# Kernel optimization log

Hardware: AMD Instinct MI355X
Metric: run time of the kernel (lower is better)

## Reference

```python
import jax, jax.numpy as jnp
import numpy as np

B, S, D = 1, 2048, 2048      # batch, seq, hidden_dim
DF = 768                      # moe intermediate (per routed expert)
DSH = 2048                    # shared-expert intermediate
E, K = 32, 8                  # num routed experts, top_k
BLK = 128                     # fp8 block-scale size
CAP = 1024
T = B * S


def _dequant(w, s, blk=BLK):
    # w: [E, M, N] fp8 values (stored fp32), s: [E, M/blk, N/blk] block scales
    Eh, M, N = w.shape
    Mb, Nb = s.shape[1], s.shape[2]
    return (w.reshape(Eh, Mb, blk, Nb, blk) * s[:, :, None, :, None]).reshape(Eh, M, N)


def setup_inputs() -> dict:
    key = jax.random.key(0)
    ks = jax.random.split(key, 13)
    n = lambda k, shp, sc=0.02: jax.random.normal(k, shp, jnp.float32) * sc
    u = lambda k, shp: jax.random.uniform(k, shp, jnp.float32, 0.005, 0.02)
    return {
        "hidden_states": jax.random.normal(ks[0], (B, S, D), jnp.float32),
        "router_w": n(ks[1], (E, D)),
        # raw fp8-value weights (simulated as fp32 integers-in-range values) + block scale_inv
        "wg_fp8": jax.random.normal(ks[2], (E, DF, D), jnp.float32),
        "sg": u(ks[3], (E, DF // BLK, D // BLK)),
        "wu_fp8": jax.random.normal(ks[4], (E, DF, D), jnp.float32),
        "su": u(ks[5], (E, DF // BLK, D // BLK)),
        "wd_fp8": jax.random.normal(ks[6], (E, D, DF), jnp.float32),
        "sd": u(ks[7], (E, D // BLK, DF // BLK)),
        "ws_gate": n(ks[8], (DSH, D)),
        "ws_up": n(ks[9], (DSH, D)),
        "ws_down": n(ks[10], (D, DSH)),
        "w_shared_gate": n(ks[11], (1, D)),
    }


def reference(hidden_states, router_w, wg_fp8, sg, wu_fp8, su, wd_fp8, sd,
              ws_gate, ws_up, ws_down, w_shared_gate):
    x = hidden_states.reshape(-1, D)  # [T, D]

    # shared expert (SwiGLU) + its sigmoid gate
    shared = (jax.nn.silu(x @ ws_gate.T) * (x @ ws_up.T)) @ ws_down.T
    sh_gate = jax.nn.sigmoid(x @ w_shared_gate.T)  # [T, 1]

    # router: softmax -> top-k -> renormalize (Qwen MoE gate)
    probs = jax.nn.softmax(x @ router_w.T, axis=-1)          # [T, E]
    rw, sel = jax.lax.top_k(probs, K)                        # [T, K]
    rw = rw / jnp.sum(rw, axis=-1, keepdims=True)

    # capacity-based dispatch (replaces the python per-expert loop; same math)
    flat_e = sel.reshape(-1)                                 # [T*K]
    oh = jax.nn.one_hot(flat_e, E, dtype=jnp.int32)
    pos = jnp.sum(jnp.cumsum(oh, axis=0) * oh, axis=-1) - 1  # position within expert
    keep = (pos < CAP)
    pos_c = jnp.minimum(pos, CAP)                            # overflow -> scratch slot CAP
    tok = jnp.arange(T * K) // K                             # owning token of each (t,k) pair

    buf = jnp.zeros((E, CAP + 1, D), x.dtype).at[flat_e, pos_c].set(x[tok])

    # block-scale dequant (fp8*scale_inv), then per-expert SwiGLU
    Wg = _dequant(wg_fp8, sg)
    Wu = _dequant(wu_fp8, su)
    Wd = _dequant(wd_fp8, sd)
    g = jnp.einsum('ecd,efd->ecf', buf, Wg)
    up = jnp.einsum('ecd,efd->ecf', buf, Wu)
    h = jax.nn.silu(g) * up
    y = jnp.einsum('ecf,edf->ecd', h, Wd)                    # [E, CAP+1, D]

    # weighted scatter-add back to tokens (index_add_ equivalent)
    y_tok = y[flat_e, pos_c]                                 # [T*K, D]
    w_tok = rw.reshape(-1) * keep.astype(x.dtype)
    out = jax.ops.segment_sum(y_tok * w_tok[:, None], tok, num_segments=T)

    out = out + sh_gate * shared
    return out.reshape(B, S, D)
```

## Files before the change

### kernel.cpp

```cpp
#include <hip/hip_runtime.h>
#include <hip/hip_bf16.h>


#define TT   2048
#define DD   2048
#define DFF  768
#define DSH  2048
#define EE   32
#define KTOP 8
#define CAP  1024

typedef _Float16 half8  __attribute__((ext_vector_type(8)));
typedef _Float16 half4v __attribute__((ext_vector_type(4)));
typedef float    f32x4  __attribute__((ext_vector_type(4)));

__global__ __launch_bounds__(256) void k_init(int* __restrict__ cnt,
                                              int* __restrict__ slot_tok) {
  int i = blockIdx.x * 256 + threadIdx.x;
  if (i < EE * CAP) slot_tok[i] = 0;
  if (i < EE) cnt[i] = 0;
}

__global__ __launch_bounds__(256) void k_cast(const float* __restrict__ in,
                                              _Float16* __restrict__ out) {
  int i = blockIdx.x * 256 + threadIdx.x;
  float4 v = ((const float4*)in)[i];
  half4v h = { (_Float16)v.x, (_Float16)v.y, (_Float16)v.z, (_Float16)v.w };
  ((half4v*)out)[i] = h;
}

__global__ __launch_bounds__(64) void k_router(
    const float* __restrict__ x, const float* __restrict__ rw,
    const float* __restrict__ wshg,
    float* __restrict__ shg, int* __restrict__ cnt,
    int* __restrict__ slot_tok, float* __restrict__ slot_w,
    int* __restrict__ slot_pair, int* __restrict__ pair_pos) {
  int t = blockIdx.x;
  int lane = threadIdx.x;
  const float* xr = x + (size_t)t * DD;
  float xv[32];
#pragma unroll
  for (int j = 0; j < 32; ++j) xv[j] = xr[lane + j * 64];

  __shared__ float lg[EE];
  for (int e = 0; e < EE; ++e) {
    const float* we = rw + (size_t)e * DD;
    float s = 0.f;
#pragma unroll
    for (int j = 0; j < 32; ++j) s += xv[j] * we[lane + j * 64];
#pragma unroll
    for (int off = 32; off > 0; off >>= 1) s += __shfl_down(s, off);
    if (lane == 0) lg[e] = s;
  }
  {
    float s = 0.f;
#pragma unroll
    for (int j = 0; j < 32; ++j) s += xv[j] * wshg[lane + j * 64];
#pragma unroll
    for (int off = 32; off > 0; off >>= 1) s += __shfl_down(s, off);
    if (lane == 0) shg[t] = 1.f / (1.f + expf(-s));
  }
  if (lane == 0) {
    unsigned used = 0;
    int sel[KTOP];
    float val[KTOP];
    for (int k = 0; k < KTOP; ++k) {
      float bv = -1e30f; int bi = 0;
      for (int e = 0; e < EE; ++e)
        if (!((used >> e) & 1) && lg[e] > bv) { bv = lg[e]; bi = e; }
      used |= (1u << bi);
      sel[k] = bi; val[k] = bv;
    }
    float mx = val[0], sum = 0.f;
    for (int k = 0; k < KTOP; ++k) { val[k] = expf(val[k] - mx); sum += val[k]; }
    float inv = 1.f / sum;
    for (int k = 0; k < KTOP; ++k) {
      int e = sel[k];
      int pos = atomicAdd(&cnt[e], 1);
      pair_pos[t * KTOP + k] = pos;
      if (pos < CAP) {
        slot_tok[e * CAP + pos] = t;
        slot_w[e * CAP + pos] = val[k] * inv;
        slot_pair[e * CAP + pos] = t * KTOP + k;
      }
    }
  }
}

template<bool DUAL, bool GATHER, bool DEQ, int EPI, int NPB, int MBB, int KDIM>
__global__ __launch_bounds__(256, 2) void k_gemm(
    const _Float16* __restrict__ A,
    const float* __restrict__ B0f, const float* __restrict__ B1f,
    const float* __restrict__ S0, const float* __restrict__ S1,
    int sCols, int sStrideE,
    _Float16* __restrict__ OutH, float* __restrict__ OutF,
    const float* __restrict__ shg,
    int ldA, int ldOut,
    long long strideAE, long long strideBE, long long strideOE,
    const int* __restrict__ cnt, int rowsConst,
    const int* __restrict__ slot_tok, const float* __restrict__ slot_w) {
  constexpr int BK = 64;
  constexpr int KT = KDIM / BK;
  constexpr int NF = DUAL ? 2 : 4;
  constexpr int BN = DUAL ? 64 : 128;
  constexpr int BCH = DUAL ? 4 : 8;

  const int f = blockIdx.x;
  const int xcd = f & 7;
  const int t0 = f >> 3;
  const int mb = t0 % MBB;
  const int pp = t0 / MBB;
  const int p  = pp * 8 + xcd;
  const int nb = p % NPB;
  const int e  = p / NPB;

  int rows = cnt ? (cnt[e] > CAP ? CAP : cnt[e]) : rowsConst;
  const int rowBase = mb * 128;
  if (rowBase >= rows) return;
  const int nBase = nb * BN;

  const int tid = threadIdx.x;
  const int lane = tid & 63;
  const int wave = tid >> 6;
  const int wr = wave >> 1;
  const int wc = wave & 1;

  __shared__ __align__(16) _Float16 sA[3][8192];
  __shared__ __align__(16) _Float16 sB[2][8192];

  const _Float16* Ae = A + (GATHER ? 0 : (long long)e * strideAE);
  const float* B0e = B0f + (long long)e * strideBE;
  const float* B1e = DUAL ? (B1f + (long long)e * strideBE) : nullptr;
  const float* S0e = DEQ ? (S0 + (long long)e * sStrideE) : nullptr;
  const float* S1e = (DEQ && DUAL) ? (S1 + (long long)e * sStrideE) : nullptr;
  const int sRow = DEQ ? (nBase >> 7) * sCols : 0;

  int aByte[4];
#pragma unroll
  for (int i = 0; i < 4; ++i) {
    int c = tid + i * 256;
    int row = c >> 3;
    int colB = ((c & 7) << 4) ^ ((row & 7) << 4);
    int src = GATHER ? slot_tok[e * CAP + rowBase + row] : (rowBase + row);
    aByte[i] = src * (2 * ldA) + colB;
  }
  int bOff[BCH], wByte[BCH];
#pragma unroll
  for (int i = 0; i < BCH; ++i) {
    int c = tid + i * 256;
    int rn = c >> 4;
    int c4 = (c & 15) << 2;
    bOff[i] = (nBase + rn) * KDIM + c4;
    wByte[i] = ((rn << 7) + (c4 << 1)) ^ ((rn & 7) << 4);
  }

  f32x4 accG[4][NF];
  f32x4 accU[DUAL ? 4 : 1][NF];
#pragma unroll
  for (int m = 0; m < 4; ++m)
#pragma unroll
    for (int n = 0; n < NF; ++n) {
      accG[m][n] = (f32x4){0.f, 0.f, 0.f, 0.f};
      if constexpr (DUAL) accU[m][n] = (f32x4){0.f, 0.f, 0.f, 0.f};
    }

  auto stageA = [&](int kt, int buf) {
#pragma unroll
    for (int i = 0; i < 4; ++i) {
      __builtin_amdgcn_global_load_lds(
          (const __attribute__((address_space(1))) void*)
              ((const char*)Ae + aByte[i] + kt * (BK * 2)),
          (__attribute__((address_space(3))) void*)&sA[buf][(tid + i * 256) * 8],
          16, 0, 0);
    }
  };
  auto loadB = [&](int kt, float4 (&r0)[BCH], float4 (&r1)[BCH]) {
    const int ko = kt * BK;
#pragma unroll
    for (int i = 0; i < BCH; ++i) r0[i] = *(const float4*)(B0e + bOff[i] + ko);
    if constexpr (DUAL) {
#pragma unroll
      for (int i = 0; i < BCH; ++i) r1[i] = *(const float4*)(B1e + bOff[i] + ko);
    }
  };
  auto storeB = [&](int kt, float4 (&r0)[BCH], float4 (&r1)[BCH]) {
    float s0 = 1.f, s1 = 1.f;
    if constexpr (DEQ) {
      s0 = S0e[sRow + (kt >> 1)];
      if constexpr (DUAL) s1 = S1e[sRow + (kt >> 1)];
    }
    char* base = (char*)&sB[kt & 1][0];
#pragma unroll
    for (int i = 0; i < BCH; ++i) {
      half4v h = { (_Float16)(r0[i].x * s0), (_Float16)(r0[i].y * s0),
                   (_Float16)(r0[i].z * s0), (_Float16)(r0[i].w * s0) };
      *(half4v*)(base + wByte[i]) = h;
      if constexpr (DUAL) {
        half4v h1 = { (_Float16)(r1[i].x * s1), (_Float16)(r1[i].y * s1),
                      (_Float16)(r1[i].z * s1), (_Float16)(r1[i].w * s1) };
        *(half4v*)(base + 8192 + wByte[i]) = h1;
      }
    }
  };
  auto computeTile = [&](int ia, int ib) {
    const char* pA = (const char*)&sA[ia][0];
    const char* pB = (const char*)&sB[ib][0];
#pragma unroll
    for (int kk = 0; kk < 2; ++kk) {
      const int koff = kk * 32 + (lane >> 4) * 8;
      half8 a[4];
#pragma unroll
      for (int m = 0; m < 4; ++m) {
        int r = wr * 64 + m * 16 + (lane & 15);
        int byt = ((r << 7) + (koff << 1)) ^ ((r & 7) << 4);
        a[m] = *(const half8*)(pA + byt);
      }
      if constexpr (DUAL) {
        half8 bg[2], bu[2];
#pragma unroll
        for (int n = 0; n < 2; ++n) {
          int rn = wc * 32 + n * 16 + (lane & 15);
          int byt = ((rn << 7) + (koff << 1)) ^ ((rn & 7) << 4);
          bg[n] = *(const half8*)(pB + byt);
          bu[n] = *(const half8*)(pB + 8192 + byt);
        }
#pragma unroll
        for (int m = 0; m < 4; ++m)
#pragma unroll
          for (int n = 0; n < 2; ++n) {
            accG[m][n] = __builtin_amdgcn_mfma_f32_16x16x32_f16(a[m], bg[n], accG[m][n], 0, 0, 0);
            accU[m][n] = __builtin_amdgcn_mfma_f32_16x16x32_f16(a[m], bu[n], accU[m][n], 0, 0, 0);
          }
      } else {
        half8 b[4];
#pragma unroll
        for (int n = 0; n < 4; ++n) {
          int rn = wc * 64 + n * 16 + (lane & 15);
          int byt = ((rn << 7) + (koff << 1)) ^ ((rn & 7) << 4);
          b[n] = *(const half8*)(pB + byt);
        }
#pragma unroll
        for (int m = 0; m < 4; ++m)
#pragma unroll
          for (int n = 0; n < 4; ++n)
            accG[m][n] = __builtin_amdgcn_mfma_f32_16x16x32_f16(a[m], b[n], accG[m][n], 0, 0, 0);
      }
    }
  };

  float4 rbE0[BCH], rbE1[BCH], rbO0[BCH], rbO1[BCH];

  stageA(0, 0); loadB(0, rbE0, rbE1);
  __builtin_amdgcn_sched_barrier(0);
  stageA(1, 1); loadB(1, rbO0, rbO1);
  __builtin_amdgcn_sched_barrier(0);

  int bufC = 0;
  int bufW = 2;

  for (int kt = 0; kt < KT; kt += 2) {
    if (kt + 1 < KT) { asm volatile("s_waitcnt vmcnt(12)" ::: "memory"); }
    else             { asm volatile("s_waitcnt vmcnt(0)"  ::: "memory"); }
    __builtin_amdgcn_sched_barrier(0);
    storeB(kt, rbE0, rbE1);
    asm volatile("s_waitcnt lgkmcnt(0)" ::: "memory");
    __builtin_amdgcn_sched_barrier(0);
    __builtin_amdgcn_s_barrier();
    __builtin_amdgcn_sched_barrier(0);
    if (kt + 2 < KT) { stageA(kt + 2, bufW); loadB(kt + 2, rbE0, rbE1); }
    __builtin_amdgcn_sched_barrier(0);
    computeTile(bufC, 0);
    bufC = (bufC == 2) ? 0 : bufC + 1;
    bufW = (bufW == 2) ? 0 : bufW + 1;

    if (kt + 2 < KT) { asm volatile("s_waitcnt vmcnt(12)" ::: "memory"); }
    else             { asm volatile("s_waitcnt vmcnt(0)"  ::: "memory"); }
    __builtin_amdgcn_sched_barrier(0);
    storeB(kt + 1, rbO0, rbO1);
    asm volatile("s_waitcnt lgkmcnt(0)" ::: "memory");
    __builtin_amdgcn_sched_barrier(0);
    __builtin_amdgcn_s_barrier();
    __builtin_amdgcn_sched_barrier(0);
    if (kt + 3 < KT) { stageA(kt + 3, bufW); loadB(kt + 3, rbO0, rbO1); }
    __builtin_amdgcn_sched_barrier(0);
    computeTile(bufC, 1);
    bufC = (bufC == 2) ? 0 : bufC + 1;
    bufW = (bufW == 2) ? 0 : bufW + 1;
  }

#pragma unroll
  for (int m = 0; m < 4; ++m) {
#pragma unroll
    for (int i = 0; i < 4; ++i) {
      int row = rowBase + wr * 64 + m * 16 + (lane >> 4) * 4 + i;
      if (row < rows) {
        if constexpr (EPI == 1) {
          int pair = slot_tok[e * CAP + row];
          float w = slot_w[e * CAP + row];
#pragma unroll
          for (int n = 0; n < NF; ++n) {
            int col = nBase + wc * 64 + n * 16 + (lane & 15);
            OutH[(long long)pair * DD + col] = (_Float16)(w * accG[m][n][i]);
          }
        } else if constexpr (EPI == 2) {
          float g = shg[row];
#pragma unroll
          for (int n = 0; n < NF; ++n) {
            int col = nBase + wc * 64 + n * 16 + (lane & 15);
            long long o = (long long)row * DD + col;
            OutF[o] += g * accG[m][n][i];
          }
        } else {
          long long outBase = (long long)e * strideOE;
#pragma unroll
          for (int n = 0; n < NF; ++n) {
            int col = nBase + (DUAL ? wc * 32 : wc * 64) + n * 16 + (lane & 15);
            long long o = outBase + (long long)row * ldOut + col;
            if constexpr (DUAL) {
              float gv = accG[m][n][i];
              float uv = accU[m][n][i];
              OutH[o] = (_Float16)((gv / (1.f + __expf(-gv))) * uv);
            } else {
              OutH[o] = (_Float16)accG[m][n][i];
            }
          }
        }
      }
    }
  }
}

__global__ __launch_bounds__(256) void k_combine(
    const _Float16* __restrict__ Yp, const int* __restrict__ pair_pos,
    float* __restrict__ out) {
  int t = blockIdx.x;
  int col = threadIdx.x * 8;
  float acc[8] = {0.f, 0.f, 0.f, 0.f, 0.f, 0.f, 0.f, 0.f};
#pragma unroll
  for (int k = 0; k < KTOP; ++k) {
    if (pair_pos[t * KTOP + k] < CAP) {
      half8 y = *(const half8*)&Yp[((size_t)t * KTOP + k) * DD + col];
#pragma unroll
      for (int j = 0; j < 8; ++j) acc[j] += (float)y[j];
    }
  }
  float4 o0 = {acc[0], acc[1], acc[2], acc[3]};
  float4 o1 = {acc[4], acc[5], acc[6], acc[7]};
  *(float4*)&out[(size_t)t * DD + col] = o0;
  *(float4*)&out[(size_t)t * DD + col + 4] = o1;
}

extern "C" void kernel_launch(void* const* d_in, const int* in_sizes, int n_in,
                              void* d_out, int out_size, void* d_ws, size_t ws_size,
                              hipStream_t stream) {
  (void)in_sizes; (void)n_in; (void)out_size; (void)ws_size;
  const float* x    = (const float*)d_in[0];
  const float* rw   = (const float*)d_in[1];
  const float* wg   = (const float*)d_in[2];
  const float* sg   = (const float*)d_in[3];
  const float* wu   = (const float*)d_in[4];
  const float* su   = (const float*)d_in[5];
  const float* wd   = (const float*)d_in[6];
  const float* sd   = (const float*)d_in[7];
  const float* wsg  = (const float*)d_in[8];
  const float* wsu  = (const float*)d_in[9];
  const float* wsd  = (const float*)d_in[10];
  const float* wshg = (const float*)d_in[11];
  float* out = (float*)d_out;

  char* p = (char*)d_ws;
  auto alloc = [&](size_t bytes) {
    char* r = p;
    p += (bytes + 255) & ~(size_t)255;
    return r;
  };
  _Float16* x_h   = (_Float16*)alloc((size_t)TT * DD * 2);
  _Float16* H     = (_Float16*)alloc((size_t)EE * CAP * DFF * 2);
  _Float16* Hsh   = (_Float16*)alloc((size_t)TT * DSH * 2);
  _Float16* Yp    = (_Float16*)alloc((size_t)TT * KTOP * DD * 2);
  float* shg      = (float*)alloc((size_t)TT * 4);
  int* cnt        = (int*)alloc((size_t)EE * 4);
  int* slot_tok   = (int*)alloc((size_t)EE * CAP * 4);
  float* slot_w   = (float*)alloc((size_t)EE * CAP * 4);
  int* slot_pair  = (int*)alloc((size_t)EE * CAP * 4);
  int* pair_pos   = (int*)alloc((size_t)TT * KTOP * 4);

  k_init<<<(EE * CAP + 255) / 256, 256, 0, stream>>>(cnt, slot_tok);
  k_cast<<<(TT * DD / 4) / 256, 256, 0, stream>>>(x, x_h);
  k_router<<<TT, 64, 0, stream>>>(x, rw, wshg, shg, cnt, slot_tok, slot_w,
                                  slot_pair, pair_pos);

  k_gemm<true, true, true, 0, 12, 8, DD><<<3072, 256, 0, stream>>>(
      x_h, wg, wu, sg, su, DD / 128, (DFF / 128) * (DD / 128),
      H, nullptr, nullptr,
      DD, DFF,
      0LL, (long long)DFF * DD, (long long)CAP * DFF,
      cnt, 0, slot_tok, nullptr);

  k_gemm<false, false, true, 1, 16, 8, DFF><<<4096, 256, 0, stream>>>(
      H, wd, wd, sd, sd, DFF / 128, (DD / 128) * (DFF / 128),
      Yp, nullptr, nullptr,
      DFF, DD,
      (long long)CAP * DFF, (long long)DD * DFF, 0LL,
      cnt, 0, slot_pair, slot_w);

  k_combine<<<TT, 256, 0, stream>>>(Yp, pair_pos, out);

  k_gemm<true, false, false, 0, 32, 16, DD><<<512, 256, 0, stream>>>(
      x_h, wsg, wsu, nullptr, nullptr, 0, 0,
      Hsh, nullptr, nullptr,
      DD, DSH,
      0LL, 0LL, 0LL,
      nullptr, TT, nullptr, nullptr);

  k_gemm<false, false, false, 2, 16, 16, DSH><<<256, 256, 0, stream>>>(
      Hsh, wsd, wsd, nullptr, nullptr, 0, 0,
      nullptr, out, shg,
      DSH, DD,
      0LL, 0LL, 0LL,
      nullptr, TT, nullptr, nullptr);
}
```

Measured before the change: 680.4 us.

## Pre-dequantize expert weights to fp16 and use direct-to-LDS GEMM path

When the workspace is large enough, separate kernels first dequantize the routed-expert weights and cast the shared-expert weights to fp16 buffers. A new GEMM kernel then streams both A and B straight into LDS with global_load_lds, so the in-loop fp32 load, scale and convert of B goes away. Each call now does extra full passes over the fp32 weights plus fp16 writes and reads, trading that traffic for a lighter GEMM mainloop. The path only runs if ws_size is at least about 270 MB; otherwise the old path is kept.

```diff
diff --git a/kernel.cpp b/kernel.cpp
--- a/kernel.cpp
+++ b/kernel.cpp
@@ -27,6 +27,19 @@
   float4 v = ((const float4*)in)[i];
   half4v h = { (_Float16)v.x, (_Float16)v.y, (_Float16)v.z, (_Float16)v.w };
   ((half4v*)out)[i] = h;
+}
+
+template<int NCOLS>
+__global__ void k_deq_row(const float* __restrict__ w, const float* __restrict__ s,
+                          int mRows, _Float16* __restrict__ outp) {
+  int r = blockIdx.x, e = blockIdx.y;
+  int c4 = threadIdx.x;
+  long long base = ((long long)e * mRows + r) * NCOLS;
+  float sc = s[(e * (mRows >> 7) + (r >> 7)) * (NCOLS >> 7) + (c4 >> 5)];
+  float4 v = ((const float4*)(w + base))[c4];
+  half4v h = { (_Float16)(v.x * sc), (_Float16)(v.y * sc),
+               (_Float16)(v.z * sc), (_Float16)(v.w * sc) };
+  ((half4v*)(outp + base))[c4] = h;
 }
 
 __global__ __launch_bounds__(64) void k_router(
@@ -82,6 +95,207 @@
         slot_tok[e * CAP + pos] = t;
         slot_w[e * CAP + pos] = val[k] * inv;
         slot_pair[e * CAP + pos] = t * KTOP + k;
+      }
+    }
+  }
+}
+
+template<bool DUAL, bool GATHER, int EPI, int NPB, int MBB, int KDIM>
+__global__ __launch_bounds__(256, 2) void k_gemm16(
+    const _Float16* __restrict__ A,
+    const _Float16* __restrict__ B0h, const _Float16* __restrict__ B1h,
+    _Float16* __restrict__ OutH, float* __restrict__ OutF,
+    const float* __restrict__ shg,
+    int ldA, int ldOut,
+    long long strideAE, long long strideBE, long long strideOE,
+    const int* __restrict__ cnt, int rowsConst,
+    const int* __restrict__ slot_tok, const float* __restrict__ slot_w) {
+  constexpr int BK = 64;
+  constexpr int KT = KDIM / BK;
+  constexpr int NF = DUAL ? 2 : 4;
+  constexpr int BN = DUAL ? 64 : 128;
+
+  const int f = blockIdx.x;
+  const int xcd = f & 7;
+  const int t0 = f >> 3;
+  const int mb = t0 % MBB;
+  const int pp = t0 / MBB;
+  const int p  = pp * 8 + xcd;
+  const int nb = p % NPB;
+  const int e  = p / NPB;
+
+  int rows = cnt ? (cnt[e] > CAP ? CAP : cnt[e]) : rowsConst;
+  const int rowBase = mb * 128;
+  if (rowBase >= rows) return;
+  const int nBase = nb * BN;
+
+  const int tid = threadIdx.x;
+  const int lane = tid & 63;
+  const int wave = tid >> 6;
+  const int wr = wave >> 1;
+  const int wc = wave & 1;
+
+  __shared__ __align__(16) _Float16 sA[3][8192];
+  __shared__ __align__(16) _Float16 sB[2][8192];
+
+  const _Float16* Ae = A + (GATHER ? 0 : (long long)e * strideAE);
+  const _Float16* B0e = B0h + (long long)e * strideBE;
+  const _Float16* B1e = DUAL ? (B1h + (long long)e * strideBE) : nullptr;
+
+  int aByte[4];
+#pragma unroll
+  for (int i = 0; i < 4; ++i) {
+    int c = tid + i * 256;
+    int row = c >> 3;
+    int colB = ((c & 7) << 4) ^ ((row & 7) << 4);
+    int src = GATHER ? slot_tok[e * CAP + rowBase + row] : (rowBase + row);
+    aByte[i] = src * (2 * ldA) + colB;
+  }
+  int bByte[4];
+#pragma unroll
+  for (int i = 0; i < 4; ++i) {
+    int c = tid + i * 256;
+    int rn = DUAL ? ((c & 511) >> 3) : (c >> 3);
+    int colB = ((c & 7) << 4) ^ ((rn & 7) << 4);
+    bByte[i] = (nBase + rn) * (2 * KDIM) + colB;
+  }
+
+  f32x4 accG[4][NF];
+  f32x4 accU[DUAL ? 4 : 1][NF];
+#pragma unroll
+  for (int m = 0; m < 4; ++m)
+#pragma unroll
+    for (int n = 0; n < NF; ++n) {
+      accG[m][n] = (f32x4){0.f, 0.f, 0.f, 0.f};
+      if constexpr (DUAL) accU[m][n] = (f32x4){0.f, 0.f, 0.f, 0.f};
+    }
+
+  auto stageA = [&](int kt, int buf) {
+#pragma unroll
+    for (int i = 0; i < 4; ++i) {
+      __builtin_amdgcn_global_load_lds(
+          (const __attribute__((address_space(1))) void*)
+              ((const char*)Ae + aByte[i] + kt * 128),
+          (__attribute__((address_space(3))) void*)&sA[buf][(tid + i * 256) * 8],
+          16, 0, 0);
+    }
+  };
+  auto stageB = [&](int kt, int buf) {
+#pragma unroll
+    for (int i = 0; i < 4; ++i) {
+      const _Float16* src = (DUAL && i >= 2) ? B1e : B0e;
+      __builtin_amdgcn_global_load_lds(
+          (const __attribute__((address_space(1))) void*)
+              ((const char*)src + bByte[i] + kt * 128),
+          (__attribute__((address_space(3))) void*)&sB[buf][(tid + i * 256) * 8],
+          16, 0, 0);
+    }
+  };
+  auto computeTile = [&](int ia, int ib) {
+    const char* pA = (const char*)&sA[ia][0];
+    const char* pB = (const char*)&sB[ib][0];
+#pragma unroll
+    for (int kk = 0; kk < 2; ++kk) {
+      const int koff = kk * 32 + (lane >> 4) * 8;
+      half8 a[4];
+#pragma unroll
+      for (int m = 0; m < 4; ++m) {
+        int r = wr * 64 + m * 16 + (lane & 15);
+        int byt = ((r << 7) + (koff << 1)) ^ ((r & 7) << 4);
+        a[m] = *(const half8*)(pA + byt);
+      }
+      if constexpr (DUAL) {
+        half8 bg[2], bu[2];
+#pragma unroll
+        for (int n = 0; n < 2; ++n) {
+          int rn = wc * 32 + n * 16 + (lane & 15);
+          int byt = ((rn << 7) + (koff << 1)) ^ ((rn & 7) << 4);
+          bg[n] = *(const half8*)(pB + byt);
+          bu[n] = *(const half8*)(pB + 8192 + byt);
+        }
+#pragma unroll
+        for (int m = 0; m < 4; ++m)
+#pragma unroll
+          for (int n = 0; n < 2; ++n) {
+            accG[m][n] = __builtin_amdgcn_mfma_f32_16x16x32_f16(a[m], bg[n], accG[m][n], 0, 0, 0);
+            accU[m][n] = __builtin_amdgcn_mfma_f32_16x16x32_f16(a[m], bu[n], accU[m][n], 0, 0, 0);
+          }
+      } else {
+        half8 b[4];
+#pragma unroll
+        for (int n = 0; n < 4; ++n) {
+          int rn = wc * 64 + n * 16 + (lane & 15);
+          int byt = ((rn << 7) + (koff << 1)) ^ ((rn & 7) << 4);
+          b[n] = *(const half8*)(pB + byt);
+        }
+#pragma unroll
+        for (int m = 0; m < 4; ++m)
+#pragma unroll
+          for (int n = 0; n < 4; ++n)
+            accG[m][n] = __builtin_amdgcn_mfma_f32_16x16x32_f16(a[m], b[n], accG[m][n], 0, 0, 0);
+      }
+    }
+  };
+
+  stageB(0, 0);
+  __builtin_amdgcn_sched_barrier(0);
+  stageA(0, 0);
+  __builtin_amdgcn_sched_barrier(0);
+  stageA(1, 1);
+  __builtin_amdgcn_sched_barrier(0);
+
+  int bufC = 0, bufW = 2;
+  for (int kt = 0; kt < KT; ++kt) {
+    asm volatile("s_waitcnt lgkmcnt(0)" ::: "memory");
+    if (kt + 1 < KT) { asm volatile("s_waitcnt vmcnt(4)" ::: "memory"); }
+    else             { asm volatile("s_waitcnt vmcnt(0)" ::: "memory"); }
+    __builtin_amdgcn_sched_barrier(0);
+    __builtin_amdgcn_s_barrier();
+    __builtin_amdgcn_sched_barrier(0);
+    if (kt + 1 < KT) stageB(kt + 1, (kt + 1) & 1);
+    if (kt + 2 < KT) stageA(kt + 2, bufW);
+    __builtin_amdgcn_sched_barrier(0);
+    computeTile(bufC, kt & 1);
+    bufC = (bufC == 2) ? 0 : bufC + 1;
+    bufW = (bufW == 2) ? 0 : bufW + 1;
+  }
+
+#pragma unroll
+  for (int m = 0; m < 4; ++m) {
+#pragma unroll
+    for (int i = 0; i < 4; ++i) {
+      int row = rowBase + wr * 64 + m * 16 + (lane >> 4) * 4 + i;
+      if (row < rows) {
+        if constexpr (EPI == 1) {
+          int pair = slot_tok[e * CAP + row];
+          float w = slot_w[e * CAP + row];
+#pragma unroll
+          for (int n = 0; n < NF; ++n) {
+            int col = nBase + wc * 64 + n * 16 + (lane & 15);
+            OutH[(long long)pair * DD + col] = (_Float16)(w * accG[m][n][i]);
+          }
+        } else if constexpr (EPI == 2) {
+          float g = shg[row];
+#pragma unroll
+          for (int n = 0; n < NF; ++n) {
+            int col = nBase + wc * 64 + n * 16 + (lane & 15);
+            OutF[(long long)row * DD + col] += g * accG[m][n][i];
+          }
+        } else {
+          long long outBase = (long long)e * strideOE;
+#pragma unroll
+          for (int n = 0; n < NF; ++n) {
+            int col = nBase + (DUAL ? wc * 32 : wc * 64) + n * 16 + (lane & 15);
+            long long o = outBase + (long long)row * ldOut + col;
+            if constexpr (DUAL) {
+              float gv = accG[m][n][i];
+              float uv = accU[m][n][i];
+              OutH[o] = (_Float16)((gv / (1.f + __expf(-gv))) * uv);
+            } else {
+              OutH[o] = (_Float16)accG[m][n][i];
+            }
+          }
+        }
       }
     }
   }
@@ -255,8 +469,7 @@
   stageA(1, 1); loadB(1, rbO0, rbO1);
   __builtin_amdgcn_sched_barrier(0);
 
-  int bufC = 0;
-  int bufW = 2;
+  int bufC = 0, bufW = 2;
 
   for (int kt = 0; kt < KT; kt += 2) {
     if (kt + 1 < KT) { asm volatile("s_waitcnt vmcnt(12)" ::: "memory"); }
@@ -307,8 +520,7 @@
 #pragma unroll
           for (int n = 0; n < NF; ++n) {
             int col = nBase + wc * 64 + n * 16 + (lane & 15);
-            long long o = (long long)row * DD + col;
-            OutF[o] += g * accG[m][n][i];
+            OutF[(long long)row * DD + col] += g * accG[m][n][i];
           }
         } else {
           long long outBase = (long long)e * strideOE;
@@ -353,7 +565,7 @@
 extern "C" void kernel_launch(void* const* d_in, const int* in_sizes, int n_in,
                               void* d_out, int out_size, void* d_ws, size_t ws_size,
                               hipStream_t stream) {
-  (void)in_sizes; (void)n_in; (void)out_size; (void)ws_size;
+  (void)in_sizes; (void)n_in; (void)out_size;
   const float* x    = (const float*)d_in[0];
   const float* rw   = (const float*)d_in[1];
   const float* wg   = (const float*)d_in[2];
@@ -374,49 +586,102 @@
     p += (bytes + 255) & ~(size_t)255;
     return r;
   };
-  _Float16* x_h   = (_Float16*)alloc((size_t)TT * DD * 2);
-  _Float16* H     = (_Float16*)alloc((size_t)EE * CAP * DFF * 2);
-  _Float16* Hsh   = (_Float16*)alloc((size_t)TT * DSH * 2);
-  _Float16* Yp    = (_Float16*)alloc((size_t)TT * KTOP * DD * 2);
-  float* shg      = (float*)alloc((size_t)TT * 4);
-  int* cnt        = (int*)alloc((size_t)EE * 4);
-  int* slot_tok   = (int*)alloc((size_t)EE * CAP * 4);
-  float* slot_w   = (float*)alloc((size_t)EE * CAP * 4);
-  int* slot_pair  = (int*)alloc((size_t)EE * CAP * 4);
-  int* pair_pos   = (int*)alloc((size_t)TT * KTOP * 4);
-
-  k_init<<<(EE * CAP + 255) / 256, 256, 0, stream>>>(cnt, slot_tok);
-  k_cast<<<(TT * DD / 4) / 256, 256, 0, stream>>>(x, x_h);
-  k_router<<<TT, 64, 0, stream>>>(x, rw, wshg, shg, cnt, slot_tok, slot_w,
-                                  slot_pair, pair_pos);
-
-  k_gemm<true, true, true, 0, 12, 8, DD><<<3072, 256, 0, stream>>>(
-      x_h, wg, wu, sg, su, DD / 128, (DFF / 128) * (DD / 128),
-      H, nullptr, nullptr,
-      DD, DFF,
-      0LL, (long long)DFF * DD, (long long)CAP * DFF,
-      cnt, 0, slot_tok, nullptr);
-
-  k_gemm<false, false, true, 1, 16, 8, DFF><<<4096, 256, 0, stream>>>(
-      H, wd, wd, sd, sd, DFF / 128, (DD / 128) * (DFF / 128),
-      Yp, nullptr, nullptr,
-      DFF, DD,
-      (long long)CAP * DFF, (long long)DD * DFF, 0LL,
-      cnt, 0, slot_pair, slot_w);
-
-  k_combine<<<TT, 256, 0, stream>>>(Yp, pair_pos, out);
-
-  k_gemm<true, false, false, 0, 32, 16, DD><<<512, 256, 0, stream>>>(
-      x_h, wsg, wsu, nullptr, nullptr, 0, 0,
-      Hsh, nullptr, nullptr,
-      DD, DSH,
-      0LL, 0LL, 0LL,
-      nullptr, TT, nullptr, nullptr);
-
-  k_gemm<false, false, false, 2, 16, 16, DSH><<<256, 256, 0, stream>>>(
-      Hsh, wsd, wsd, nullptr, nullptr, 0, 0,
-      nullptr, out, shg,
-      DSH, DD,
-      0LL, 0LL, 0LL,
-      nullptr, TT, nullptr, nullptr);
-}
+
+  const bool big = ws_size >= (size_t)270 * 1000 * 1000;
+
+  if (big) {
+    _Float16* x_h  = (_Float16*)alloc((size_t)TT * DD * 2);
+    _Float16* bufA = (_Float16*)alloc((size_t)EE * DFF * DD * 2);
+    _Float16* bufB = (_Float16*)alloc((size_t)EE * DFF * DD * 2);
+    _Float16* bufH = (_Float16*)alloc((size_t)EE * CAP * DFF * 2);
+    _Float16* Hsh  = (_Float16*)alloc((size_t)TT * DSH * 2);
+    float* shg     = (float*)alloc((size_t)TT * 4);
+    int* cnt       = (int*)alloc((size_t)EE * 4);
+    int* slot_tok  = (int*)alloc((size_t)EE * CAP * 4);
+    float* slot_w  = (float*)alloc((size_t)EE * CAP * 4);
+    int* slot_pair = (int*)alloc((size_t)EE * CAP * 4);
+    int* pair_pos  = (int*)alloc((size_t)TT * KTOP * 4);
+
+    _Float16* Yp    = bufB;
+    _Float16* wsg_h = bufH;
+    _Float16* wsu_h = bufH + (size_t)TT * DD;
+    _Float16* wsd_h = bufH + (size_t)2 * TT * DD;
+
+    k_init<<<(EE * CAP + 255) / 256, 256, 0, stream>>>(cnt, slot_tok);
+    k_cast<<<(TT * DD / 4) / 256, 256, 0, stream>>>(x, x_h);
+    k_router<<<TT, 64, 0, stream>>>(x, rw, wshg, shg, cnt, slot_tok, slot_w,
+                                    slot_pair, pair_pos);
+
+    k_deq_row<DD><<<dim3(DFF, EE), DD / 4, 0, stream>>>(wg, sg, DFF, bufA);
+    k_deq_row<DD><<<dim3(DFF, EE), DD / 4, 0, stream>>>(wu, su, DFF, bufB);
+
+    k_gemm16<true, true, 0, 12, 8, DD><<<3072, 256, 0, stream>>>(
+        x_h, bufA, bufB, bufH, nullptr, nullptr,
+        DD, DFF, 0LL, (long long)DFF * DD, (long long)CAP * DFF,
+        cnt, 0, slot_tok, nullptr);
+
+    k_deq_row<DFF><<<dim3(DD, EE), DFF / 4, 0, stream>>>(wd, sd, DD, bufA);
+    k_gemm16<false, false, 1, 16, 8, DFF><<<4096, 256, 0, stream>>>(
+        bufH, bufA, bufA, Yp, nullptr, nullptr,
+        DFF, DD, (long long)CAP * DFF, (long long)DD * DFF, 0LL,
+        cnt, 0, slot_pair, slot_w);
+
+    k_combine<<<TT, 256, 0, stream>>>(Yp, pair_pos, out);
+
+    k_cast<<<(DD * DSH / 4) / 256, 256, 0, stream>>>(wsg, wsg_h);
+    k_cast<<<(DD * DSH / 4) / 256, 256, 0, stream>>>(wsu, wsu_h);
+    k_cast<<<(DD * DSH / 4) / 256, 256, 0, stream>>>(wsd, wsd_h);
+
+    k_gemm16<true, false, 0, 32, 16, DD><<<512, 256, 0, stream>>>(
+        x_h, wsg_h, wsu_h, Hsh, nullptr, nullptr,
+        DD, DSH, 0LL, 0LL, 0LL,
+        nullptr, TT, nullptr, nullptr);
+
+    k_gemm16<false, false, 2, 16, 16, DSH><<<256, 256, 0, stream>>>(
+        Hsh, wsd_h, wsd_h, nullptr, out, shg,
+        DSH, DD, 0LL, 0LL, 0LL,
+        nullptr, TT, nullptr, nullptr);
+  } else {
+    _Float16* x_h   = (_Float16*)alloc((size_t)TT * DD * 2);
+    _Float16* H     = (_Float16*)alloc((size_t)EE * CAP * DFF * 2);
+    _Float16* Hsh   = (_Float16*)alloc((size_t)TT * DSH * 2);
+    _Float16* Yp    = (_Float16*)alloc((size_t)TT * KTOP * DD * 2);
+    float* shg      = (float*)alloc((size_t)TT * 4);
+    int* cnt        = (int*)alloc((size_t)EE * 4);
+    int* slot_tok   = (int*)alloc((size_t)EE * CAP * 4);
+    float* slot_w   = (float*)alloc((size_t)EE * CAP * 4);
+    int* slot_pair  = (int*)alloc((size_t)EE * CAP * 4);
+    int* pair_pos   = (int*)alloc((size_t)TT * KTOP * 4);
+
+    k_init<<<(EE * CAP + 255) / 256, 256, 0, stream>>>(cnt, slot_tok);
+    k_cast<<<(TT * DD / 4) / 256, 256, 0, stream>>>(x, x_h);
+    k_router<<<TT, 64, 0, stream>>>(x, rw, wshg, shg, cnt, slot_tok, slot_w,
+                                    slot_pair, pair_pos);
+
+    k_gemm<true, true, true, 0, 12, 8, DD><<<3072, 256, 0, stream>>>(
+        x_h, wg, wu, sg, su, DD / 128, (DFF / 128) * (DD / 128),
+        H, nullptr, nullptr,
+        DD, DFF, 0LL, (long long)DFF * DD, (long long)CAP * DFF,
+        cnt, 0, slot_tok, nullptr);
+
+    k_gemm<false, false, true, 1, 16, 8, DFF><<<4096, 256, 0, stream>>>(
+        H, wd, wd, sd, sd, DFF / 128, (DD / 128) * (DFF / 128),
+        Yp, nullptr, nullptr,
+        DFF, DD, (long long)CAP * DFF, (long long)DD * DFF, 0LL,
+        cnt, 0, slot_pair, slot_w);
+
+    k_combine<<<TT, 256, 0, stream>>>(Yp, pair_pos, out);
+
+    k_gemm<true, false, false, 0, 32, 16, DD><<<512, 256, 0, stream>>>(
+        x_h, wsg, wsu, nullptr, nullptr, 0, 0,
+        Hsh, nullptr, nullptr,
+        DD, DSH, 0LL, 0LL, 0LL,
+        nullptr, TT, nullptr, nullptr);
+
+    k_gemm<false, false, false, 2, 16, 16, DSH><<<256, 256, 0, stream>>>(
+        Hsh, wsd, wsd, nullptr, nullptr, 0, 0,
+        nullptr, out, shg,
+        DSH, DD, 0LL, 0LL, 0LL,
+        nullptr, TT, nullptr, nullptr);
+  }
+}
```

New measurement: 747.3 us. 9.8% more time.

## Add specialized gate/up expert GEMM with register-resident dequantized B operands

Applied to the files above, without the earlier changes.

Replaces the generic templated kernel for the routed-expert gate/up GEMM with a dedicated kernel. Each wave stages its own gathered A rows into per-wave LDS buffers, which removes block-wide barriers. The fp32 fp8-valued weights are loaded straight into registers and converted to fp16 with their block scales, rather than going through shared memory. The next tiles' loads are issued in the middle of the current MFMA tile to overlap memory with compute. In exchange, register pressure is much higher (two sets of 16 float4 buffers), which risks lower occupancy or spills. B fragments are also no longer shared across waves through LDS, so global weight traffic per block goes up.

```diff
diff --git a/kernel.cpp b/kernel.cpp
--- a/kernel.cpp
+++ b/kernel.cpp
@@ -82,6 +82,191 @@
         slot_tok[e * CAP + pos] = t;
         slot_w[e * CAP + pos] = val[k] * inv;
         slot_pair[e * CAP + pos] = t * KTOP + k;
+      }
+    }
+  }
+}
+
+template<int NPB, int MBB>
+__global__ __launch_bounds__(256, 2) void k_guwf(
+    const _Float16* __restrict__ A,
+    const float* __restrict__ B0f, const float* __restrict__ B1f,
+    const float* __restrict__ S0, const float* __restrict__ S1,
+    int sCols, int sStrideE,
+    _Float16* __restrict__ OutH,
+    int ldA, int ldOut, long long strideBE, long long strideOE,
+    const int* __restrict__ cnt, const int* __restrict__ slot_tok) {
+  constexpr int KDIM = DD;
+  constexpr int KT = KDIM / 64;
+
+  const int f = blockIdx.x;
+  const int xcd = f & 7;
+  const int t0 = f >> 3;
+  const int mb = t0 % MBB;
+  const int pp = t0 / MBB;
+  const int p  = pp * 8 + xcd;
+  const int nb = p % NPB;
+  const int e  = p / NPB;
+
+  const int tid = threadIdx.x;
+
+  int rows = cnt[e] > CAP ? CAP : cnt[e];
+  const int rowBase = mb * 128;
+  if (rowBase >= rows) return;
+  const int nBase = nb * 64;
+
+  const int lane = tid & 63;
+  const int wave = tid >> 6;
+  const int wr = wave >> 1;
+  const int wc = wave & 1;
+
+  __shared__ __align__(16) _Float16 sAw[4][2][4096];
+  __shared__ float sSc[2][16];
+
+  {
+    const int sRow = (nBase >> 7) * sCols;
+    if (tid < 16)       sSc[0][tid]      = S0[(long long)e * sStrideE + sRow + tid];
+    else if (tid < 32)  sSc[1][tid - 16] = S1[(long long)e * sStrideE + sRow + (tid - 16)];
+  }
+  __syncthreads();
+
+  const float* B0e = B0f + (long long)e * strideBE;
+  const float* B1e = B1f + (long long)e * strideBE;
+
+  int aByte[8];
+#pragma unroll
+  for (int i = 0; i < 8; ++i) {
+    int c = lane + i * 64;
+    int lr = c >> 3;
+    int colB = ((c & 7) << 4) ^ ((lr & 7) << 4);
+    int grow = rowBase + wr * 64 + lr;
+    int src = slot_tok[e * CAP + grow];
+    aByte[i] = src * (2 * ldA) + colB;
+  }
+  int bOffs[4];
+#pragma unroll
+  for (int kk = 0; kk < 2; ++kk)
+#pragma unroll
+    for (int n = 0; n < 2; ++n) {
+      int rn = nBase + wc * 32 + n * 16 + (lane & 15);
+      bOffs[kk * 2 + n] = rn * KDIM + kk * 32 + (lane >> 4) * 8;
+    }
+
+  f32x4 accG[4][2], accU[4][2];
+#pragma unroll
+  for (int m = 0; m < 4; ++m)
+#pragma unroll
+    for (int n = 0; n < 2; ++n) {
+      accG[m][n] = (f32x4){0.f, 0.f, 0.f, 0.f};
+      accU[m][n] = (f32x4){0.f, 0.f, 0.f, 0.f};
+    }
+
+  auto stageA = [&](int kt, int buf) {
+#pragma unroll
+    for (int i = 0; i < 8; ++i) {
+      __builtin_amdgcn_global_load_lds(
+          (const __attribute__((address_space(1))) void*)
+              ((const char*)A + aByte[i] + kt * 128),
+          (__attribute__((address_space(3))) void*)
+              &sAw[wave][buf][(lane + i * 64) * 8],
+          16, 0, 0);
+    }
+  };
+  auto loadB = [&](int kt, float4 (&r)[16]) {
+    const int ko = kt * 64;
+#pragma unroll
+    for (int kk = 0; kk < 2; ++kk)
+#pragma unroll
+      for (int o = 0; o < 2; ++o)
+#pragma unroll
+        for (int n = 0; n < 2; ++n) {
+          const float* src = o ? B1e : B0e;
+          const float* q = src + bOffs[kk * 2 + n] + ko;
+          int idx = ((kk * 2 + o) * 2 + n) * 2;
+          r[idx]     = *(const float4*)q;
+          r[idx + 1] = *(const float4*)(q + 4);
+        }
+  };
+
+  auto tile = [&](int t, float4 (&r)[16]) {
+    const char* pA = (const char*)&sAw[wave][t & 1][0];
+    float s0 = sSc[0][t >> 1];
+    float s1 = sSc[1][t >> 1];
+#pragma unroll
+    for (int kk = 0; kk < 2; ++kk) {
+      half8 hg[2], hu[2];
+#pragma unroll
+      for (int o = 0; o < 2; ++o)
+#pragma unroll
+        for (int n = 0; n < 2; ++n) {
+          int idx = ((kk * 2 + o) * 2 + n) * 2;
+          float4 lo = r[idx], hi = r[idx + 1];
+          float s = o ? s1 : s0;
+          half8 h = { (_Float16)(lo.x * s), (_Float16)(lo.y * s),
+                      (_Float16)(lo.z * s), (_Float16)(lo.w * s),
+                      (_Float16)(hi.x * s), (_Float16)(hi.y * s),
+                      (_Float16)(hi.z * s), (_Float16)(hi.w * s) };
+          if (o) hu[n] = h; else hg[n] = h;
+        }
+      if (kk == 1 && t + 2 < KT) {
+        loadB(t + 2, r);
+        __builtin_amdgcn_sched_barrier(0);
+      }
+      const int koffB = kk * 64 + (lane >> 4) * 16;
+      half8 a[4];
+#pragma unroll
+      for (int m = 0; m < 4; ++m) {
+        int lr = m * 16 + (lane & 15);
+        int byt = (lr << 7) + (koffB ^ ((lr & 7) << 4));
+        a[m] = *(const half8*)(pA + byt);
+      }
+      if (kk == 1) {
+        asm volatile("s_waitcnt lgkmcnt(0)" ::: "memory");
+        __builtin_amdgcn_sched_barrier(0);
+        if (t + 2 < KT) stageA(t + 2, t & 1);
+        __builtin_amdgcn_sched_barrier(0);
+      }
+#pragma unroll
+      for (int m = 0; m < 4; ++m)
+#pragma unroll
+        for (int n = 0; n < 2; ++n) {
+          accG[m][n] = __builtin_amdgcn_mfma_f32_16x16x32_f16(a[m], hg[n], accG[m][n], 0, 0, 0);
+          accU[m][n] = __builtin_amdgcn_mfma_f32_16x16x32_f16(a[m], hu[n], accU[m][n], 0, 0, 0);
+        }
+    }
+  };
+
+  float4 rE[16], rO[16];
+
+  loadB(0, rE);  stageA(0, 0);
+  loadB(1, rO);  stageA(1, 1);
+  __builtin_amdgcn_sched_barrier(0);
+
+  for (int t = 0; t < KT; t += 2) {
+    if (t + 1 < KT) { asm volatile("s_waitcnt vmcnt(24)" ::: "memory"); }
+    else            { asm volatile("s_waitcnt vmcnt(0)"  ::: "memory"); }
+    __builtin_amdgcn_sched_barrier(0);
+    tile(t, rE);
+    if (t + 2 < KT) { asm volatile("s_waitcnt vmcnt(24)" ::: "memory"); }
+    else            { asm volatile("s_waitcnt vmcnt(0)"  ::: "memory"); }
+    __builtin_amdgcn_sched_barrier(0);
+    tile(t + 1, rO);
+  }
+
+#pragma unroll
+  for (int m = 0; m < 4; ++m) {
+#pragma unroll
+    for (int i = 0; i < 4; ++i) {
+      int row = rowBase + wr * 64 + m * 16 + (lane >> 4) * 4 + i;
+      if (row < rows) {
+#pragma unroll
+        for (int n = 0; n < 2; ++n) {
+          int col = nBase + wc * 32 + n * 16 + (lane & 15);
+          float gv = accG[m][n][i];
+          float uv = accU[m][n][i];
+          OutH[(long long)e * strideOE + (long long)row * ldOut + col] =
+              (_Float16)((gv / (1.f + __expf(-gv))) * uv);
+        }
       }
     }
   }
@@ -255,8 +440,7 @@
   stageA(1, 1); loadB(1, rbO0, rbO1);
   __builtin_amdgcn_sched_barrier(0);
 
-  int bufC = 0;
-  int bufW = 2;
+  int bufC = 0, bufW = 2;
 
   for (int kt = 0; kt < KT; kt += 2) {
     if (kt + 1 < KT) { asm volatile("s_waitcnt vmcnt(12)" ::: "memory"); }
@@ -307,8 +491,7 @@
 #pragma unroll
           for (int n = 0; n < NF; ++n) {
             int col = nBase + wc * 64 + n * 16 + (lane & 15);
-            long long o = (long long)row * DD + col;
-            OutF[o] += g * accG[m][n][i];
+            OutF[(long long)row * DD + col] += g * accG[m][n][i];
           }
         } else {
           long long outBase = (long long)e * strideOE;
@@ -390,12 +573,10 @@
   k_router<<<TT, 64, 0, stream>>>(x, rw, wshg, shg, cnt, slot_tok, slot_w,
                                   slot_pair, pair_pos);
 
-  k_gemm<true, true, true, 0, 12, 8, DD><<<3072, 256, 0, stream>>>(
+  k_guwf<12, 8><<<3072, 256, 0, stream>>>(
       x_h, wg, wu, sg, su, DD / 128, (DFF / 128) * (DD / 128),
-      H, nullptr, nullptr,
-      DD, DFF,
-      0LL, (long long)DFF * DD, (long long)CAP * DFF,
-      cnt, 0, slot_tok, nullptr);
+      H, DD, DFF, (long long)DFF * DD, (long long)CAP * DFF,
+      cnt, slot_tok);
 
   k_gemm<false, false, true, 1, 16, 8, DFF><<<4096, 256, 0, stream>>>(
       H, wd, wd, sd, sd, DFF / 128, (DD / 128) * (DFF / 128),
```

Result: slower. 1.704 ms (+150.4%).

## Merge routed and shared expert GEMMs into combined launches, fuse cast into router

Applied to the files above, without the earlier changes.

The separate fp32-to-fp16 cast kernel is folded into the router, which already loads each token row. The routed gate/up GEMM and the shared gate/up GEMM now run as one launch with block-index dispatch, and the same is done for the two down projections. The shared down-projection result goes to an fp16 buffer, and a single combine kernel adds the gated shared output to the routed sum. This cuts launch count and lets the small shared GEMMs fill tail gaps left by the routed grid, at the cost of an extra fp16 intermediate write and read and fp16 rounding of the shared output.

```diff
diff --git a/kernel.cpp b/kernel.cpp
--- a/kernel.cpp
+++ b/kernel.cpp
@@ -21,17 +21,10 @@
   if (i < EE) cnt[i] = 0;
 }
 
-__global__ __launch_bounds__(256) void k_cast(const float* __restrict__ in,
-                                              _Float16* __restrict__ out) {
-  int i = blockIdx.x * 256 + threadIdx.x;
-  float4 v = ((const float4*)in)[i];
-  half4v h = { (_Float16)v.x, (_Float16)v.y, (_Float16)v.z, (_Float16)v.w };
-  ((half4v*)out)[i] = h;
-}
-
 __global__ __launch_bounds__(64) void k_router(
     const float* __restrict__ x, const float* __restrict__ rw,
     const float* __restrict__ wshg,
+    _Float16* __restrict__ x_h,
     float* __restrict__ shg, int* __restrict__ cnt,
     int* __restrict__ slot_tok, float* __restrict__ slot_w,
     int* __restrict__ slot_pair, int* __restrict__ pair_pos) {
@@ -41,6 +34,10 @@
   float xv[32];
 #pragma unroll
   for (int j = 0; j < 32; ++j) xv[j] = xr[lane + j * 64];
+
+#pragma unroll
+  for (int j = 0; j < 32; ++j)
+    x_h[(size_t)t * DD + lane + j * 64] = (_Float16)xv[j];
 
   __shared__ float lg[EE];
   for (int e = 0; e < EE; ++e) {
@@ -87,37 +84,19 @@
   }
 }
 
-template<bool DUAL, bool GATHER, bool DEQ, int EPI, int NPB, int MBB, int KDIM>
-__global__ __launch_bounds__(256, 2) void k_gemm(
-    const _Float16* __restrict__ A,
-    const float* __restrict__ B0f, const float* __restrict__ B1f,
-    const float* __restrict__ S0, const float* __restrict__ S1,
-    int sCols, int sStrideE,
-    _Float16* __restrict__ OutH, float* __restrict__ OutF,
-    const float* __restrict__ shg,
-    int ldA, int ldOut,
-    long long strideAE, long long strideBE, long long strideOE,
-    const int* __restrict__ cnt, int rowsConst,
-    const int* __restrict__ slot_tok, const float* __restrict__ slot_w) {
+template<bool DUAL, bool GATHER, bool DEQ, int EPI, int KDIM>
+__device__ __forceinline__ void gemm_body(
+    _Float16 (*sA)[8192], _Float16 (*sB)[8192],
+    const _Float16* __restrict__ Ae,
+    const float* __restrict__ B0e, const float* __restrict__ B1e,
+    const float* __restrict__ S0e, const float* __restrict__ S1e, int sRow,
+    _Float16* __restrict__ OutH, long long outBase, int ldOut,
+    int ldA, int rows, int rowBase, int nBase,
+    const int* __restrict__ slotBase, const float* __restrict__ slotW) {
   constexpr int BK = 64;
   constexpr int KT = KDIM / BK;
   constexpr int NF = DUAL ? 2 : 4;
-  constexpr int BN = DUAL ? 64 : 128;
   constexpr int BCH = DUAL ? 4 : 8;
-
-  const int f = blockIdx.x;
-  const int xcd = f & 7;
-  const int t0 = f >> 3;
-  const int mb = t0 % MBB;
-  const int pp = t0 / MBB;
-  const int p  = pp * 8 + xcd;
-  const int nb = p % NPB;
-  const int e  = p / NPB;
-
-  int rows = cnt ? (cnt[e] > CAP ? CAP : cnt[e]) : rowsConst;
-  const int rowBase = mb * 128;
-  if (rowBase >= rows) return;
-  const int nBase = nb * BN;
 
   const int tid = threadIdx.x;
   const int lane = tid & 63;
@@ -125,23 +104,13 @@
   const int wr = wave >> 1;
   const int wc = wave & 1;
 
-  __shared__ __align__(16) _Float16 sA[3][8192];
-  __shared__ __align__(16) _Float16 sB[2][8192];
-
-  const _Float16* Ae = A + (GATHER ? 0 : (long long)e * strideAE);
-  const float* B0e = B0f + (long long)e * strideBE;
-  const float* B1e = DUAL ? (B1f + (long long)e * strideBE) : nullptr;
-  const float* S0e = DEQ ? (S0 + (long long)e * sStrideE) : nullptr;
-  const float* S1e = (DEQ && DUAL) ? (S1 + (long long)e * sStrideE) : nullptr;
-  const int sRow = DEQ ? (nBase >> 7) * sCols : 0;
-
   int aByte[4];
 #pragma unroll
   for (int i = 0; i < 4; ++i) {
     int c = tid + i * 256;
     int row = c >> 3;
     int colB = ((c & 7) << 4) ^ ((row & 7) << 4);
-    int src = GATHER ? slot_tok[e * CAP + rowBase + row] : (rowBase + row);
+    int src = GATHER ? slotBase[rowBase + row] : (rowBase + row);
     aByte[i] = src * (2 * ldA) + colB;
   }
   int bOff[BCH], wByte[BCH];
@@ -295,23 +264,14 @@
       int row = rowBase + wr * 64 + m * 16 + (lane >> 4) * 4 + i;
       if (row < rows) {
         if constexpr (EPI == 1) {
-          int pair = slot_tok[e * CAP + row];
-          float w = slot_w[e * CAP + row];
+          int pair = slotBase[row];
+          float w = slotW[row];
 #pragma unroll
           for (int n = 0; n < NF; ++n) {
             int col = nBase + wc * 64 + n * 16 + (lane & 15);
             OutH[(long long)pair * DD + col] = (_Float16)(w * accG[m][n][i]);
           }
-        } else if constexpr (EPI == 2) {
-          float g = shg[row];
-#pragma unroll
-          for (int n = 0; n < NF; ++n) {
-            int col = nBase + wc * 64 + n * 16 + (lane & 15);
-            long long o = (long long)row * DD + col;
-            OutF[o] += g * accG[m][n][i];
-          }
         } else {
-          long long outBase = (long long)e * strideOE;
 #pragma unroll
           for (int n = 0; n < NF; ++n) {
             int col = nBase + (DUAL ? wc * 32 : wc * 64) + n * 16 + (lane & 15);
@@ -330,12 +290,100 @@
   }
 }
 
-__global__ __launch_bounds__(256) void k_combine(
-    const _Float16* __restrict__ Yp, const int* __restrict__ pair_pos,
+__global__ __launch_bounds__(256, 2) void k_gu(
+    const _Float16* __restrict__ x_h,
+    const float* __restrict__ wg, const float* __restrict__ wu,
+    const float* __restrict__ sg, const float* __restrict__ su,
+    _Float16* __restrict__ H,
+    const float* __restrict__ wsg, const float* __restrict__ wsu,
+    _Float16* __restrict__ Hsh,
+    const int* __restrict__ cnt, const int* __restrict__ slot_tok) {
+  __shared__ __align__(16) _Float16 sA[3][8192];
+  __shared__ __align__(16) _Float16 sB[2][8192];
+  const int bid = blockIdx.x;
+  if (bid < 3072) {
+    const int xcd = bid & 7, t0 = bid >> 3;
+    const int mb = t0 % 8, pp = t0 / 8;
+    const int p = pp * 8 + xcd;
+    const int nb = p % 12, e = p / 12;
+    int rows = cnt[e] > CAP ? CAP : cnt[e];
+    const int rowBase = mb * 128;
+    if (rowBase >= rows) return;
+    gemm_body<true, true, true, 0, DD>(
+        sA, sB, x_h,
+        wg + (long long)e * DFF * DD, wu + (long long)e * DFF * DD,
+        sg + (long long)e * ((DFF / 128) * (DD / 128)),
+        su + (long long)e * ((DFF / 128) * (DD / 128)),
+        ((nb * 64) >> 7) * (DD / 128),
+        H, (long long)e * CAP * DFF, DFF,
+        DD, rows, rowBase, nb * 64,
+        slot_tok + e * CAP, nullptr);
+  } else {
+    const int f = bid - 3072;
+    const int xcd = f & 7, t0 = f >> 3;
+    const int mb = t0 % 16, pp = t0 / 16;
+    const int nb = pp * 8 + xcd;
+    gemm_body<true, false, false, 0, DD>(
+        sA, sB, x_h,
+        wsg, wsu, nullptr, nullptr, 0,
+        Hsh, 0LL, DSH,
+        DD, TT, mb * 128, nb * 64,
+        nullptr, nullptr);
+  }
+}
+
+__global__ __launch_bounds__(256, 2) void k_dn(
+    const _Float16* __restrict__ H,
+    const float* __restrict__ wd, const float* __restrict__ sd,
+    _Float16* __restrict__ Yp,
+    const _Float16* __restrict__ Hsh, const float* __restrict__ wsd,
+    _Float16* __restrict__ Ysh,
+    const int* __restrict__ cnt,
+    const int* __restrict__ slot_pair, const float* __restrict__ slot_w) {
+  __shared__ __align__(16) _Float16 sA[3][8192];
+  __shared__ __align__(16) _Float16 sB[2][8192];
+  const int bid = blockIdx.x;
+  if (bid < 4096) {
+    const int xcd = bid & 7, t0 = bid >> 3;
+    const int mb = t0 % 8, pp = t0 / 8;
+    const int p = pp * 8 + xcd;
+    const int nb = p % 16, e = p / 16;
+    int rows = cnt[e] > CAP ? CAP : cnt[e];
+    const int rowBase = mb * 128;
+    if (rowBase >= rows) return;
+    gemm_body<false, false, true, 1, DFF>(
+        sA, sB, H + (long long)e * CAP * DFF,
+        wd + (long long)e * DD * DFF, wd + (long long)e * DD * DFF,
+        sd + (long long)e * ((DD / 128) * (DFF / 128)), nullptr,
+        ((nb * 128) >> 7) * (DFF / 128),
+        Yp, 0LL, DD,
+        DFF, rows, rowBase, nb * 128,
+        slot_pair + e * CAP, slot_w + e * CAP);
+  } else {
+    const int f = bid - 4096;
+    const int xcd = f & 7, t0 = f >> 3;
+    const int mb = t0 % 16, pp = t0 / 16;
+    const int nb = pp * 8 + xcd;
+    gemm_body<false, false, false, 0, DSH>(
+        sA, sB, Hsh,
+        wsd, wsd, nullptr, nullptr, 0,
+        Ysh, 0LL, DD,
+        DSH, TT, mb * 128, nb * 128,
+        nullptr, nullptr);
+  }
+}
+
+__global__ __launch_bounds__(256) void k_combine2(
+    const _Float16* __restrict__ Yp, const _Float16* __restrict__ Ysh,
+    const float* __restrict__ shg, const int* __restrict__ pair_pos,
     float* __restrict__ out) {
   int t = blockIdx.x;
   int col = threadIdx.x * 8;
-  float acc[8] = {0.f, 0.f, 0.f, 0.f, 0.f, 0.f, 0.f, 0.f};
+  float acc[8];
+  half8 ys = *(const half8*)&Ysh[(size_t)t * DD + col];
+  float g = shg[t];
+#pragma unroll
+  for (int j = 0; j < 8; ++j) acc[j] = g * (float)ys[j];
 #pragma unroll
   for (int k = 0; k < KTOP; ++k) {
     if (pair_pos[t * KTOP + k] < CAP) {
@@ -378,6 +426,7 @@
   _Float16* H     = (_Float16*)alloc((size_t)EE * CAP * DFF * 2);
   _Float16* Hsh   = (_Float16*)alloc((size_t)TT * DSH * 2);
   _Float16* Yp    = (_Float16*)alloc((size_t)TT * KTOP * DD * 2);
+  _Float16* Ysh   = (_Float16*)alloc((size_t)TT * DD * 2);
   float* shg      = (float*)alloc((size_t)TT * 4);
   int* cnt        = (int*)alloc((size_t)EE * 4);
   int* slot_tok   = (int*)alloc((size_t)EE * CAP * 4);
@@ -386,37 +435,14 @@
   int* pair_pos   = (int*)alloc((size_t)TT * KTOP * 4);
 
   k_init<<<(EE * CAP + 255) / 256, 256, 0, stream>>>(cnt, slot_tok);
-  k_cast<<<(TT * DD / 4) / 256, 256, 0, stream>>>(x, x_h);
-  k_router<<<TT, 64, 0, stream>>>(x, rw, wshg, shg, cnt, slot_tok, slot_w,
-                                  slot_pair, pair_pos);
-
-  k_gemm<true, true, true, 0, 12, 8, DD><<<3072, 256, 0, stream>>>(
-      x_h, wg, wu, sg, su, DD / 128, (DFF / 128) * (DD / 128),
-      H, nullptr, nullptr,
-      DD, DFF,
-      0LL, (long long)DFF * DD, (long long)CAP * DFF,
-      cnt, 0, slot_tok, nullptr);
-
-  k_gemm<false, false, true, 1, 16, 8, DFF><<<4096, 256, 0, stream>>>(
-      H, wd, wd, sd, sd, DFF / 128, (DD / 128) * (DFF / 128),
-      Yp, nullptr, nullptr,
-      DFF, DD,
-      (long long)CAP * DFF, (long long)DD * DFF, 0LL,
-      cnt, 0, slot_pair, slot_w);
-
-  k_combine<<<TT, 256, 0, stream>>>(Yp, pair_pos, out);
-
-  k_gemm<true, false, false, 0, 32, 16, DD><<<512, 256, 0, stream>>>(
-      x_h, wsg, wsu, nullptr, nullptr, 0, 0,
-      Hsh, nullptr, nullptr,
-      DD, DSH,
-      0LL, 0LL, 0LL,
-      nullptr, TT, nullptr, nullptr);
-
-  k_gemm<false, false, false, 2, 16, 16, DSH><<<256, 256, 0, stream>>>(
-      Hsh, wsd, wsd, nullptr, nullptr, 0, 0,
-      nullptr, out, shg,
-      DSH, DD,
-      0LL, 0LL, 0LL,
-      nullptr, TT, nullptr, nullptr);
-}
+  k_router<<<TT, 64, 0, stream>>>(x, rw, wshg, x_h, shg, cnt, slot_tok,
+                                  slot_w, slot_pair, pair_pos);
+
+  k_gu<<<3584, 256, 0, stream>>>(x_h, wg, wu, sg, su, H, wsg, wsu, Hsh,
+                                 cnt, slot_tok);
+
+  k_dn<<<4352, 256, 0, stream>>>(H, wd, sd, Yp, Hsh, wsd, Ysh,
+                                 cnt, slot_pair, slot_w);
+
+  k_combine2<<<TT, 256, 0, stream>>>(Yp, Ysh, shg, pair_pos, out);
+}
```

After: 655.0 us (median of 2 runs). 3.7% less time.
